# Kernel optimization log

Measured on AMD Instinct MI355X. Metric: run time of the kernel, lower is better.

Reference implementation:

```python
import jax, jax.numpy as jnp
import numpy as np
from jax import lax

N, C, A, H, W = 32, 512, 256, 64, 64

def _maxpool2(t):
    # 2x2 max pool, stride 2, NCHW
    return lax.reduce_window(t, -jnp.inf, lax.max, (1, 1, 2, 2), (1, 1, 2, 2), 'VALID')

def setup_inputs() -> dict:
    key = jax.random.key(0)
    ks = jax.random.split(key, 5)
    return {
        'x': jax.random.normal(ks[0], (N, C, H, W), dtype=jnp.float32),
        'w_g': jax.random.normal(ks[1], (A, C), dtype=jnp.float32) * 0.02,
        'b_g': jax.random.normal(ks[2], (A,), dtype=jnp.float32) * 0.02,
        'w_phi': jax.random.normal(ks[3], (A, C), dtype=jnp.float32) * 0.02,
        'b_phi': jax.random.normal(ks[4], (A,), dtype=jnp.float32) * 0.02,
    }

def reference(x, w_g, b_g, w_phi, b_phi):
    n, c, h, w = x.shape
    # g: 1x1 conv in->attn, flattened spatial: (N, A, H*W)
    g_x = (jnp.einsum('nchw,ac->nahw', x, w_g) + b_g[None, :, None, None]).reshape(n, A, h * w)
    # theta: maxpool of x, (N, C, HW/4)
    theta_x = _maxpool2(x).reshape(n, c, -1)
    # phi: 1x1 conv then maxpool, (N, HW/4, A)
    phi_conv = jnp.einsum('nchw,ac->nahw', x, w_phi) + b_phi[None, :, None, None]
    phi_x = _maxpool2(phi_conv).reshape(n, A, -1)  # (N, A, HW/4)
    # channel-attention scores: (N, C, A)
    cmat = jnp.einsum('ncm,nam->nca', theta_x, phi_x)
    attn = jax.nn.softmax(cmat, axis=-1)
    # aggregate: (N, C, HW)
    y = jnp.einsum('nca,nal->ncl', attn, g_x)
    z = y.reshape(n, c, h, w)
    return z + x
```

## Files before the change

### kernel.cpp

```cpp
#include <hip/hip_runtime.h>


typedef _Float16 half8 __attribute__((ext_vector_type(8)));
typedef _Float16 half4v __attribute__((ext_vector_type(4)));
typedef float f32x4 __attribute__((ext_vector_type(4)));

#define NB 32
#define CD 512
#define AD 256
#define PD 4096
#define PPD 1024

#define OFF_XT    0UL
#define OFF_WC    134217728UL
#define OFF_THETA 134742016UL
#define OFF_GT    168296448UL
#define OFF_PHI   235405312UL
#define OFF_ATTN  252182528UL

#define GLOAD16(gp, lp) \
    __builtin_amdgcn_global_load_lds((const __attribute__((address_space(1))) void*)(gp), \
                                     (__attribute__((address_space(3))) void*)(lp), 16, 0, 0)

__device__ __forceinline__ int swz_off(int row, int q) {
    return row * 32 + ((q ^ ((row >> 1) & 3)) * 8);
}

template <int LD>
__device__ __forceinline__ void stage2(const _Float16* __restrict__ Ab,
                                       const _Float16* __restrict__ Bb,
                                       int k0, _Float16* bufA, _Float16* bufB, int t) {
#pragma unroll
    for (int j = 0; j < 4; ++j) {
        int idx = j * 256 + t;
        int ci = idx & 511;
        int row = ci >> 2, chP = ci & 3;
        int chL = chP ^ ((row >> 1) & 3);
        const _Float16* src = ((idx < 512) ? Ab : Bb) + (size_t)row * LD + k0 + chL * 8;
        _Float16* dst = ((idx < 512) ? bufA : bufB) + ci * 8;
        GLOAD16(src, dst);
    }
}

__global__ __launch_bounds__(256) void k_prep_w(const float* __restrict__ w_g,
                                                const float* __restrict__ w_phi,
                                                _Float16* __restrict__ Wc) {
    int idx4 = blockIdx.x * 256 + threadIdx.x;
    int flat = idx4 * 4;
    const float* src = (flat < AD * CD) ? (w_g + flat) : (w_phi + (flat - AD * CD));
    float4 v = *(const float4*)src;
    half4v h;
    h[0] = (_Float16)v.x; h[1] = (_Float16)v.y; h[2] = (_Float16)v.z; h[3] = (_Float16)v.w;
    *(half4v*)(Wc + flat) = h;
}

__global__ __launch_bounds__(256) void k_prep_x(const float* __restrict__ x,
                                                _Float16* __restrict__ xT,
                                                _Float16* __restrict__ theta) {
    __shared__ _Float16 tile[32 * 136];
    int pb = blockIdx.x;
    int cb = blockIdx.y;
    int n  = blockIdx.z;
    int t  = threadIdx.x;
    int p0 = pb * 128, c0 = cb * 32;

    const float* xbase = x + ((size_t)n * CD + c0) * PD + p0;
#pragma unroll
    for (int i = 0; i < 4; ++i) {
        int idx = i * 256 + t;
        int cl = idx >> 5;
        int ch = idx & 31;
        float4 v = *(const float4*)(xbase + (size_t)cl * PD + ch * 4);
        half4v h;
        h[0] = (_Float16)v.x; h[1] = (_Float16)v.y; h[2] = (_Float16)v.z; h[3] = (_Float16)v.w;
        *(half4v*)&tile[cl * 136 + ch * 4] = h;
    }
    __syncthreads();

    {
        int pl = t >> 1, ch = t & 1;
        _Float16 vals[16] __attribute__((aligned(16)));
#pragma unroll
        for (int j = 0; j < 16; ++j) vals[j] = tile[(ch * 16 + j) * 136 + pl];
        _Float16* dst = xT + ((size_t)n * PD + p0 + pl) * CD + c0 + ch * 16;
        *(uint4*)dst       = *(uint4*)&vals[0];
        *(uint4*)(dst + 8) = *(uint4*)&vals[8];
    }
    {
        int cl = t >> 3, u0 = (t & 7) * 4;
        _Float16 o[4] __attribute__((aligned(8)));
#pragma unroll
        for (int j = 0; j < 4; ++j) {
            int w2 = (u0 + j) * 2;
            float a0 = (float)tile[cl * 136 + w2];
            float a1 = (float)tile[cl * 136 + w2 + 1];
            float a2 = (float)tile[cl * 136 + 64 + w2];
            float a3 = (float)tile[cl * 136 + 64 + w2 + 1];
            o[j] = (_Float16)fmaxf(fmaxf(a0, a1), fmaxf(a2, a3));
        }
        _Float16* dst = theta + ((size_t)n * CD + c0 + cl) * PPD + pb * 32 + u0;
        *(uint2*)dst = *(uint2*)&o[0];
    }
}

__global__ __launch_bounds__(256) void k_gemm1(const _Float16* __restrict__ Wc,
                                               const _Float16* __restrict__ xT,
                                               const float* __restrict__ b_g,
                                               const float* __restrict__ b_phi,
                                               _Float16* __restrict__ gT,
                                               _Float16* __restrict__ phi) {
    __shared__ _Float16 smem[17408];

    int pb = blockIdx.x, ab = blockIdx.y, n = blockIdx.z;
    int a0 = ab * 128, p0 = pb * 128;
    int t = threadIdx.x;
    int w = t >> 6, l = t & 63;
    int ln = l & 15, q = l >> 4;
    int mw = (w >> 1) * 64, nw = (w & 1) * 64;

    const f32x4 vzero = {0.f, 0.f, 0.f, 0.f};
    f32x4 acc[4][4];
#pragma unroll
    for (int i = 0; i < 4; ++i)
#pragma unroll
        for (int j = 0; j < 4; ++j) acc[i][j] = vzero;

    const _Float16* Abase = Wc + (size_t)a0 * CD;
    const _Float16* Bbase = xT + ((size_t)n * PD + p0) * CD;

    stage2<CD>(Abase, Bbase, 0, smem, smem + 4096, t);
    __syncthreads();

    for (int ks = 0; ks < 16; ++ks) {
        int oc = (ks & 1) << 13;
        int on = oc ^ 8192;
        if (ks < 15) stage2<CD>(Abase, Bbase, (ks + 1) * 32, smem + on, smem + on + 4096, t);
        _Float16* As = smem + oc;
        _Float16* Bs = smem + oc + 4096;
        half8 af[4], bf[4];
#pragma unroll
        for (int mt = 0; mt < 4; ++mt) af[mt] = *(const half8*)&As[swz_off(mw + mt * 16 + ln, q)];
#pragma unroll
        for (int nt = 0; nt < 4; ++nt) bf[nt] = *(const half8*)&Bs[swz_off(nw + nt * 16 + ln, q)];
#pragma unroll
        for (int mt = 0; mt < 4; ++mt)
#pragma unroll
            for (int nt = 0; nt < 4; ++nt)
                acc[mt][nt] = __builtin_amdgcn_mfma_f32_16x16x32_f16(af[mt], bf[nt], acc[mt][nt], 0, 0, 0);
        __syncthreads();
    }

    bool is_g = (a0 < 256);
    const float* bias = is_g ? b_g : b_phi;
    int abase = a0 - (is_g ? 0 : 256);
    float bv[4][4];
#pragma unroll
    for (int mt = 0; mt < 4; ++mt)
#pragma unroll
        for (int r = 0; r < 4; ++r) bv[mt][r] = bias[abase + mw + mt * 16 + q * 4 + r];

    _Float16* T = smem;
    if (is_g) {
#pragma unroll
        for (int mt = 0; mt < 4; ++mt)
#pragma unroll
            for (int nt = 0; nt < 4; ++nt)
#pragma unroll
                for (int r = 0; r < 4; ++r) {
                    int al = mw + mt * 16 + q * 4 + r;
                    int pl = nw + nt * 16 + ln;
                    T[pl * 136 + al] = (_Float16)(acc[mt][nt][r] + bv[mt][r]);
                }
        __syncthreads();
#pragma unroll
        for (int i = 0; i < 8; ++i) {
            int idx = i * 256 + t;
            int pl = idx >> 4, ch = idx & 15;
            uint4 v = *(uint4*)&T[pl * 136 + ch * 8];
            *(uint4*)(gT + ((size_t)n * PD + p0 + pl) * AD + a0 + ch * 8) = v;
        }
    } else {
#pragma unroll
        for (int mt = 0; mt < 4; ++mt)
#pragma unroll
            for (int nt = 0; nt < 4; ++nt)
#pragma unroll
                for (int r = 0; r < 4; ++r) {
                    int al = mw + mt * 16 + q * 4 + r;
                    int pl = nw + nt * 16 + ln;
                    T[al * 136 + pl] = (_Float16)(acc[mt][nt][r] + bv[mt][r]);
                }
        __syncthreads();
        int al = t >> 1, hf = t & 1;
        _Float16 o[16] __attribute__((aligned(16)));
#pragma unroll
        for (int j = 0; j < 16; ++j) {
            int u = hf * 16 + j;
            float v0 = (float)T[al * 136 + 2 * u];
            float v1 = (float)T[al * 136 + 2 * u + 1];
            float v2 = (float)T[al * 136 + 64 + 2 * u];
            float v3 = (float)T[al * 136 + 64 + 2 * u + 1];
            o[j] = (_Float16)fmaxf(fmaxf(v0, v1), fmaxf(v2, v3));
        }
        _Float16* dst = phi + ((size_t)n * AD + (a0 - 256) + al) * PPD + pb * 32 + hf * 16;
        *(uint4*)dst       = *(uint4*)&o[0];
        *(uint4*)(dst + 8) = *(uint4*)&o[8];
    }
}

__global__ __launch_bounds__(256) void k_gemm2(const _Float16* __restrict__ theta,
                                               const _Float16* __restrict__ phi,
                                               _Float16* __restrict__ attn) {
    __shared__ float red[3 * 64 * 65];
    int cb = blockIdx.x;
    int n  = blockIdx.y;
    int t = threadIdx.x, w = t >> 6, l = t & 63;
    int ln = l & 15, q = l >> 4;
    int c0 = cb * 16;

    const _Float16* Ab = theta + ((size_t)n * CD + c0 + ln) * PPD + w * 256;
    const _Float16* Bb = phi + ((size_t)n * AD + ln) * PPD + w * 256;

    const f32x4 vzero = {0.f, 0.f, 0.f, 0.f};
    f32x4 acc[16];
#pragma unroll
    for (int i = 0; i < 16; ++i) acc[i] = vzero;

    for (int k0 = 0; k0 < 256; k0 += 32) {
        half8 af = *(const half8*)(Ab + k0 + q * 8);
#pragma unroll
        for (int nt = 0; nt < 16; ++nt) {
            half8 bf = *(const half8*)(Bb + (size_t)nt * 16 * PPD + k0 + q * 8);
            acc[nt] = __builtin_amdgcn_mfma_f32_16x16x32_f16(af, bf, acc[nt], 0, 0, 0);
        }
    }

    if (w > 0) {
        float* dst = red + (w - 1) * 64 * 65 + l * 65;
#pragma unroll
        for (int nt = 0; nt < 16; ++nt)
#pragma unroll
            for (int r = 0; r < 4; ++r) dst[nt * 4 + r] = acc[nt][r];
    }
    __syncthreads();
    if (w == 0) {
#pragma unroll
        for (int j = 0; j < 3; ++j) {
            const float* src = red + j * 64 * 65 + l * 65;
#pragma unroll
            for (int nt = 0; nt < 16; ++nt)
#pragma unroll
                for (int r = 0; r < 4; ++r) acc[nt][r] += src[nt * 4 + r];
        }
#pragma unroll
        for (int r = 0; r < 4; ++r) {
            float m = -1e30f;
#pragma unroll
            for (int nt = 0; nt < 16; ++nt) m = fmaxf(m, acc[nt][r]);
#pragma unroll
            for (int s = 1; s < 16; s <<= 1) m = fmaxf(m, __shfl_xor(m, s, 64));
            float sum = 0.f;
#pragma unroll
            for (int nt = 0; nt < 16; ++nt) {
                float e = __expf(acc[nt][r] - m);
                acc[nt][r] = e;
                sum += e;
            }
#pragma unroll
            for (int s = 1; s < 16; s <<= 1) sum += __shfl_xor(sum, s, 64);
            float inv = 1.0f / sum;
            int c = c0 + q * 4 + r;
            _Float16* dst = attn + ((size_t)n * CD + c) * AD + ln;
#pragma unroll
            for (int nt = 0; nt < 16; ++nt) dst[nt * 16] = (_Float16)(acc[nt][r] * inv);
        }
    }
}

__global__ __launch_bounds__(256) void k_gemm3(const _Float16* __restrict__ attn,
                                               const _Float16* __restrict__ gT,
                                               const float* __restrict__ x,
                                               float* __restrict__ out) {
    __shared__ _Float16 smem[16384];

    int pb = blockIdx.x, cb = blockIdx.y, n = blockIdx.z;
    int c0 = cb * 128, p0 = pb * 128;
    int t = threadIdx.x;
    int w = t >> 6, l = t & 63;
    int ln = l & 15, q = l >> 4;
    int mw = (w >> 1) * 64, nw = (w & 1) * 64;

    const f32x4 vzero = {0.f, 0.f, 0.f, 0.f};
    f32x4 acc[4][4];
#pragma unroll
    for (int i = 0; i < 4; ++i)
#pragma unroll
        for (int j = 0; j < 4; ++j) acc[i][j] = vzero;

    const _Float16* Abase = attn + ((size_t)n * CD + c0) * AD;
    const _Float16* Bbase = gT + ((size_t)n * PD + p0) * AD;

    stage2<AD>(Abase, Bbase, 0, smem, smem + 4096, t);
    __syncthreads();

    for (int ks = 0; ks < 8; ++ks) {
        int oc = (ks & 1) << 13;
        int on = oc ^ 8192;
        if (ks < 7) stage2<AD>(Abase, Bbase, (ks + 1) * 32, smem + on, smem + on + 4096, t);
        _Float16* As = smem + oc;
        _Float16* Bs = smem + oc + 4096;
        half8 af[4], bf[4];
#pragma unroll
        for (int mt = 0; mt < 4; ++mt) af[mt] = *(const half8*)&Bs[swz_off(mw + mt * 16 + ln, q)];
#pragma unroll
        for (int nt = 0; nt < 4; ++nt) bf[nt] = *(const half8*)&As[swz_off(nw + nt * 16 + ln, q)];
#pragma unroll
        for (int mt = 0; mt < 4; ++mt)
#pragma unroll
            for (int nt = 0; nt < 4; ++nt)
                acc[mt][nt] = __builtin_amdgcn_mfma_f32_16x16x32_f16(af[mt], bf[nt], acc[mt][nt], 0, 0, 0);
        __syncthreads();
    }

#pragma unroll
    for (int mt = 0; mt < 4; ++mt) {
        int p = p0 + mw + mt * 16 + q * 4;
#pragma unroll
        for (int nt = 0; nt < 4; ++nt) {
            int c = c0 + nw + nt * 16 + ln;
            size_t off = ((size_t)n * CD + c) * PD + p;
            f32x4 xv = *(const f32x4*)(x + off);
            *(f32x4*)(out + off) = acc[mt][nt] + xv;
        }
    }
}

extern "C" void kernel_launch(void* const* d_in, const int* in_sizes, int n_in,
                              void* d_out, int out_size, void* d_ws, size_t ws_size,
                              hipStream_t stream) {
    const float* x     = (const float*)d_in[0];
    const float* w_g   = (const float*)d_in[1];
    const float* b_g   = (const float*)d_in[2];
    const float* w_phi = (const float*)d_in[3];
    const float* b_phi = (const float*)d_in[4];
    float* out = (float*)d_out;

    char* ws = (char*)d_ws;
    _Float16* xT    = (_Float16*)(ws + OFF_XT);
    _Float16* Wc    = (_Float16*)(ws + OFF_WC);
    _Float16* theta = (_Float16*)(ws + OFF_THETA);
    _Float16* gT    = (_Float16*)(ws + OFF_GT);
    _Float16* phi   = (_Float16*)(ws + OFF_PHI);
    _Float16* attn  = (_Float16*)(ws + OFF_ATTN);

    k_prep_w<<<dim3(256), 256, 0, stream>>>(w_g, w_phi, Wc);
    k_prep_x<<<dim3(32, 16, 32), 256, 0, stream>>>(x, xT, theta);
    k_gemm1<<<dim3(32, 4, 32), 256, 0, stream>>>(Wc, xT, b_g, b_phi, gT, phi);
    k_gemm2<<<dim3(32, 32), 256, 0, stream>>>(theta, phi, attn);
    k_gemm3<<<dim3(32, 4, 32), 256, 0, stream>>>(attn, gT, x, out);
}
```

Measured before the change: 778.6 us.

## Load GEMM operands directly from global memory instead of LDS staging

```diff
diff --git a/kernel.cpp b/kernel.cpp
--- a/kernel.cpp
+++ b/kernel.cpp
@@ -17,30 +17,6 @@
 #define OFF_GT    168296448UL
 #define OFF_PHI   235405312UL
 #define OFF_ATTN  252182528UL
-
-#define GLOAD16(gp, lp) \
-    __builtin_amdgcn_global_load_lds((const __attribute__((address_space(1))) void*)(gp), \
-                                     (__attribute__((address_space(3))) void*)(lp), 16, 0, 0)
-
-__device__ __forceinline__ int swz_off(int row, int q) {
-    return row * 32 + ((q ^ ((row >> 1) & 3)) * 8);
-}
-
-template <int LD>
-__device__ __forceinline__ void stage2(const _Float16* __restrict__ Ab,
-                                       const _Float16* __restrict__ Bb,
-                                       int k0, _Float16* bufA, _Float16* bufB, int t) {
-#pragma unroll
-    for (int j = 0; j < 4; ++j) {
-        int idx = j * 256 + t;
-        int ci = idx & 511;
-        int row = ci >> 2, chP = ci & 3;
-        int chL = chP ^ ((row >> 1) & 3);
-        const _Float16* src = ((idx < 512) ? Ab : Bb) + (size_t)row * LD + k0 + chL * 8;
-        _Float16* dst = ((idx < 512) ? bufA : bufB) + ci * 8;
-        GLOAD16(src, dst);
-    }
-}
 
 __global__ __launch_bounds__(256) void k_prep_w(const float* __restrict__ w_g,
                                                 const float* __restrict__ w_phi,
@@ -109,7 +85,7 @@
                                                const float* __restrict__ b_phi,
                                                _Float16* __restrict__ gT,
                                                _Float16* __restrict__ phi) {
-    __shared__ _Float16 smem[17408];
+    __shared__ _Float16 T[128 * 136];
 
     int pb = blockIdx.x, ab = blockIdx.y, n = blockIdx.z;
     int a0 = ab * 128, p0 = pb * 128;
@@ -125,29 +101,27 @@
 #pragma unroll
         for (int j = 0; j < 4; ++j) acc[i][j] = vzero;
 
-    const _Float16* Abase = Wc + (size_t)a0 * CD;
-    const _Float16* Bbase = xT + ((size_t)n * PD + p0) * CD;
-
-    stage2<CD>(Abase, Bbase, 0, smem, smem + 4096, t);
-    __syncthreads();
-
+    const _Float16* arow[4];
+    const _Float16* brow[4];
+#pragma unroll
+    for (int mt = 0; mt < 4; ++mt)
+        arow[mt] = Wc + (size_t)(a0 + mw + mt * 16 + ln) * CD + q * 8;
+#pragma unroll
+    for (int nt = 0; nt < 4; ++nt)
+        brow[nt] = xT + ((size_t)n * PD + p0 + nw + nt * 16 + ln) * CD + q * 8;
+
+#pragma unroll 4
     for (int ks = 0; ks < 16; ++ks) {
-        int oc = (ks & 1) << 13;
-        int on = oc ^ 8192;
-        if (ks < 15) stage2<CD>(Abase, Bbase, (ks + 1) * 32, smem + on, smem + on + 4096, t);
-        _Float16* As = smem + oc;
-        _Float16* Bs = smem + oc + 4096;
         half8 af[4], bf[4];
 #pragma unroll
-        for (int mt = 0; mt < 4; ++mt) af[mt] = *(const half8*)&As[swz_off(mw + mt * 16 + ln, q)];
-#pragma unroll
-        for (int nt = 0; nt < 4; ++nt) bf[nt] = *(const half8*)&Bs[swz_off(nw + nt * 16 + ln, q)];
+        for (int mt = 0; mt < 4; ++mt) af[mt] = *(const half8*)(arow[mt] + ks * 32);
+#pragma unroll
+        for (int nt = 0; nt < 4; ++nt) bf[nt] = *(const half8*)(brow[nt] + ks * 32);
 #pragma unroll
         for (int mt = 0; mt < 4; ++mt)
 #pragma unroll
             for (int nt = 0; nt < 4; ++nt)
                 acc[mt][nt] = __builtin_amdgcn_mfma_f32_16x16x32_f16(af[mt], bf[nt], acc[mt][nt], 0, 0, 0);
-        __syncthreads();
     }
 
     bool is_g = (a0 < 256);
@@ -159,7 +133,6 @@
 #pragma unroll
         for (int r = 0; r < 4; ++r) bv[mt][r] = bias[abase + mw + mt * 16 + q * 4 + r];
 
-    _Float16* T = smem;
     if (is_g) {
 #pragma unroll
         for (int mt = 0; mt < 4; ++mt)
@@ -281,8 +254,6 @@
                                                const _Float16* __restrict__ gT,
                                                const float* __restrict__ x,
                                                float* __restrict__ out) {
-    __shared__ _Float16 smem[16384];
-
     int pb = blockIdx.x, cb = blockIdx.y, n = blockIdx.z;
     int c0 = cb * 128, p0 = pb * 128;
     int t = threadIdx.x;
@@ -297,29 +268,27 @@
 #pragma unroll
         for (int j = 0; j < 4; ++j) acc[i][j] = vzero;
 
-    const _Float16* Abase = attn + ((size_t)n * CD + c0) * AD;
-    const _Float16* Bbase = gT + ((size_t)n * PD + p0) * AD;
-
-    stage2<AD>(Abase, Bbase, 0, smem, smem + 4096, t);
-    __syncthreads();
-
+    const _Float16* arow[4];
+    const _Float16* brow[4];
+#pragma unroll
+    for (int mt = 0; mt < 4; ++mt)
+        arow[mt] = gT + ((size_t)n * PD + p0 + mw + mt * 16 + ln) * AD + q * 8;
+#pragma unroll
+    for (int nt = 0; nt < 4; ++nt)
+        brow[nt] = attn + ((size_t)n * CD + c0 + nw + nt * 16 + ln) * AD + q * 8;
+
+#pragma unroll 4
     for (int ks = 0; ks < 8; ++ks) {
-        int oc = (ks & 1) << 13;
-        int on = oc ^ 8192;
-        if (ks < 7) stage2<AD>(Abase, Bbase, (ks + 1) * 32, smem + on, smem + on + 4096, t);
-        _Float16* As = smem + oc;
-        _Float16* Bs = smem + oc + 4096;
         half8 af[4], bf[4];
 #pragma unroll
-        for (int mt = 0; mt < 4; ++mt) af[mt] = *(const half8*)&Bs[swz_off(mw + mt * 16 + ln, q)];
-#pragma unroll
-        for (int nt = 0; nt < 4; ++nt) bf[nt] = *(const half8*)&As[swz_off(nw + nt * 16 + ln, q)];
+        for (int mt = 0; mt < 4; ++mt) af[mt] = *(const half8*)(arow[mt] + ks * 32);
+#pragma unroll
+        for (int nt = 0; nt < 4; ++nt) bf[nt] = *(const half8*)(brow[nt] + ks * 32);
 #pragma unroll
         for (int mt = 0; mt < 4; ++mt)
 #pragma unroll
             for (int nt = 0; nt < 4; ++nt)
                 acc[mt][nt] = __builtin_amdgcn_mfma_f32_16x16x32_f16(af[mt], bf[nt], acc[mt][nt], 0, 0, 0);
-        __syncthreads();
     }
 
 #pragma unroll
```

Result: slower. 940.6 us (+20.8%).

## Triple-buffer LDS staging in GEMM kernels with one barrier per k-step

Applied to the files above, without the earlier changes.

```diff
diff --git a/kernel.cpp b/kernel.cpp
--- a/kernel.cpp
+++ b/kernel.cpp
@@ -109,7 +109,7 @@
                                                const float* __restrict__ b_phi,
                                                _Float16* __restrict__ gT,
                                                _Float16* __restrict__ phi) {
-    __shared__ _Float16 smem[17408];
+    __shared__ _Float16 smem[24576];
 
     int pb = blockIdx.x, ab = blockIdx.y, n = blockIdx.z;
     int a0 = ab * 128, p0 = pb * 128;
@@ -129,12 +129,18 @@
     const _Float16* Bbase = xT + ((size_t)n * PD + p0) * CD;
 
     stage2<CD>(Abase, Bbase, 0, smem, smem + 4096, t);
-    __syncthreads();
-
-    for (int ks = 0; ks < 16; ++ks) {
-        int oc = (ks & 1) << 13;
-        int on = oc ^ 8192;
-        if (ks < 15) stage2<CD>(Abase, Bbase, (ks + 1) * 32, smem + on, smem + on + 4096, t);
+    stage2<CD>(Abase, Bbase, 32, smem + 8192, smem + 8192 + 4096, t);
+
+#pragma unroll
+    for (int ks = 0; ks < 15; ++ks) {
+        asm volatile("s_waitcnt vmcnt(4)" ::: "memory");
+        __builtin_amdgcn_s_barrier();
+        __builtin_amdgcn_sched_barrier(0);
+        if (ks + 2 < 16) {
+            int ob = ((ks + 2) % 3) * 8192;
+            stage2<CD>(Abase, Bbase, (ks + 2) * 32, smem + ob, smem + ob + 4096, t);
+        }
+        int oc = (ks % 3) * 8192;
         _Float16* As = smem + oc;
         _Float16* Bs = smem + oc + 4096;
         half8 af[4], bf[4];
@@ -147,8 +153,26 @@
 #pragma unroll
             for (int nt = 0; nt < 4; ++nt)
                 acc[mt][nt] = __builtin_amdgcn_mfma_f32_16x16x32_f16(af[mt], bf[nt], acc[mt][nt], 0, 0, 0);
-        __syncthreads();
-    }
+    }
+    asm volatile("s_waitcnt vmcnt(0)" ::: "memory");
+    __builtin_amdgcn_s_barrier();
+    __builtin_amdgcn_sched_barrier(0);
+    {
+        int oc = (15 % 3) * 8192;
+        _Float16* As = smem + oc;
+        _Float16* Bs = smem + oc + 4096;
+        half8 af[4], bf[4];
+#pragma unroll
+        for (int mt = 0; mt < 4; ++mt) af[mt] = *(const half8*)&As[swz_off(mw + mt * 16 + ln, q)];
+#pragma unroll
+        for (int nt = 0; nt < 4; ++nt) bf[nt] = *(const half8*)&Bs[swz_off(nw + nt * 16 + ln, q)];
+#pragma unroll
+        for (int mt = 0; mt < 4; ++mt)
+#pragma unroll
+            for (int nt = 0; nt < 4; ++nt)
+                acc[mt][nt] = __builtin_amdgcn_mfma_f32_16x16x32_f16(af[mt], bf[nt], acc[mt][nt], 0, 0, 0);
+    }
+    __syncthreads();
 
     bool is_g = (a0 < 256);
     const float* bias = is_g ? b_g : b_phi;
@@ -281,7 +305,7 @@
                                                const _Float16* __restrict__ gT,
                                                const float* __restrict__ x,
                                                float* __restrict__ out) {
-    __shared__ _Float16 smem[16384];
+    __shared__ _Float16 smem[24576];
 
     int pb = blockIdx.x, cb = blockIdx.y, n = blockIdx.z;
     int c0 = cb * 128, p0 = pb * 128;
@@ -301,12 +325,18 @@
     const _Float16* Bbase = gT + ((size_t)n * PD + p0) * AD;
 
     stage2<AD>(Abase, Bbase, 0, smem, smem + 4096, t);
-    __syncthreads();
-
-    for (int ks = 0; ks < 8; ++ks) {
-        int oc = (ks & 1) << 13;
-        int on = oc ^ 8192;
-        if (ks < 7) stage2<AD>(Abase, Bbase, (ks + 1) * 32, smem + on, smem + on + 4096, t);
+    stage2<AD>(Abase, Bbase, 32, smem + 8192, smem + 8192 + 4096, t);
+
+#pragma unroll
+    for (int ks = 0; ks < 7; ++ks) {
+        asm volatile("s_waitcnt vmcnt(4)" ::: "memory");
+        __builtin_amdgcn_s_barrier();
+        __builtin_amdgcn_sched_barrier(0);
+        if (ks + 2 < 8) {
+            int ob = ((ks + 2) % 3) * 8192;
+            stage2<AD>(Abase, Bbase, (ks + 2) * 32, smem + ob, smem + ob + 4096, t);
+        }
+        int oc = (ks % 3) * 8192;
         _Float16* As = smem + oc;
         _Float16* Bs = smem + oc + 4096;
         half8 af[4], bf[4];
@@ -319,18 +349,41 @@
 #pragma unroll
             for (int nt = 0; nt < 4; ++nt)
                 acc[mt][nt] = __builtin_amdgcn_mfma_f32_16x16x32_f16(af[mt], bf[nt], acc[mt][nt], 0, 0, 0);
-        __syncthreads();
+    }
+    asm volatile("s_waitcnt vmcnt(0)" ::: "memory");
+    __builtin_amdgcn_s_barrier();
+    __builtin_amdgcn_sched_barrier(0);
+    {
+        int oc = (7 % 3) * 8192;
+        _Float16* As = smem + oc;
+        _Float16* Bs = smem + oc + 4096;
+        half8 af[4], bf[4];
+#pragma unroll
+        for (int mt = 0; mt < 4; ++mt) af[mt] = *(const half8*)&Bs[swz_off(mw + mt * 16 + ln, q)];
+#pragma unroll
+        for (int nt = 0; nt < 4; ++nt) bf[nt] = *(const half8*)&As[swz_off(nw + nt * 16 + ln, q)];
+#pragma unroll
+        for (int mt = 0; mt < 4; ++mt)
+#pragma unroll
+            for (int nt = 0; nt < 4; ++nt)
+                acc[mt][nt] = __builtin_amdgcn_mfma_f32_16x16x32_f16(af[mt], bf[nt], acc[mt][nt], 0, 0, 0);
     }
 
 #pragma unroll
     for (int mt = 0; mt < 4; ++mt) {
         int p = p0 + mw + mt * 16 + q * 4;
+        size_t offs[4];
+        f32x4 xv[4];
 #pragma unroll
         for (int nt = 0; nt < 4; ++nt) {
             int c = c0 + nw + nt * 16 + ln;
-            size_t off = ((size_t)n * CD + c) * PD + p;
-            f32x4 xv = *(const f32x4*)(x + off);
-            *(f32x4*)(out + off) = acc[mt][nt] + xv;
+            offs[nt] = ((size_t)n * CD + c) * PD + p;
+            xv[nt] = __builtin_nontemporal_load((const f32x4*)(x + offs[nt]));
+        }
+#pragma unroll
+        for (int nt = 0; nt < 4; ++nt) {
+            f32x4 r = acc[mt][nt] + xv[nt];
+            __builtin_nontemporal_store(r, (f32x4*)(out + offs[nt]));
         }
     }
 }
```

Result: no change. 776.7 us (-0.2%).

## Fuse x transpose/theta pooling into first GEMM with full-K LDS panel

Applied to the files above, without the earlier changes.

```diff
diff --git a/kernel.cpp b/kernel.cpp
--- a/kernel.cpp
+++ b/kernel.cpp
@@ -11,7 +11,6 @@
 #define PD 4096
 #define PPD 1024
 
-#define OFF_XT    0UL
 #define OFF_WC    134217728UL
 #define OFF_THETA 134742016UL
 #define OFF_GT    168296448UL
@@ -54,69 +53,53 @@
     *(half4v*)(Wc + flat) = h;
 }
 
-__global__ __launch_bounds__(256) void k_prep_x(const float* __restrict__ x,
-                                                _Float16* __restrict__ xT,
-                                                _Float16* __restrict__ theta) {
-    __shared__ _Float16 tile[32 * 136];
-    int pb = blockIdx.x;
-    int cb = blockIdx.y;
-    int n  = blockIdx.z;
-    int t  = threadIdx.x;
-    int p0 = pb * 128, c0 = cb * 32;
-
-    const float* xbase = x + ((size_t)n * CD + c0) * PD + p0;
-#pragma unroll
-    for (int i = 0; i < 4; ++i) {
-        int idx = i * 256 + t;
-        int cl = idx >> 5;
-        int ch = idx & 31;
-        float4 v = *(const float4*)(xbase + (size_t)cl * PD + ch * 4);
-        half4v h;
-        h[0] = (_Float16)v.x; h[1] = (_Float16)v.y; h[2] = (_Float16)v.z; h[3] = (_Float16)v.w;
-        *(half4v*)&tile[cl * 136 + ch * 4] = h;
-    }
-    __syncthreads();
-
-    {
-        int pl = t >> 1, ch = t & 1;
-        _Float16 vals[16] __attribute__((aligned(16)));
-#pragma unroll
-        for (int j = 0; j < 16; ++j) vals[j] = tile[(ch * 16 + j) * 136 + pl];
-        _Float16* dst = xT + ((size_t)n * PD + p0 + pl) * CD + c0 + ch * 16;
-        *(uint4*)dst       = *(uint4*)&vals[0];
-        *(uint4*)(dst + 8) = *(uint4*)&vals[8];
-    }
-    {
-        int cl = t >> 3, u0 = (t & 7) * 4;
-        _Float16 o[4] __attribute__((aligned(8)));
-#pragma unroll
-        for (int j = 0; j < 4; ++j) {
-            int w2 = (u0 + j) * 2;
-            float a0 = (float)tile[cl * 136 + w2];
-            float a1 = (float)tile[cl * 136 + w2 + 1];
-            float a2 = (float)tile[cl * 136 + 64 + w2];
-            float a3 = (float)tile[cl * 136 + 64 + w2 + 1];
-            o[j] = (_Float16)fmaxf(fmaxf(a0, a1), fmaxf(a2, a3));
-        }
-        _Float16* dst = theta + ((size_t)n * CD + c0 + cl) * PPD + pb * 32 + u0;
-        *(uint2*)dst = *(uint2*)&o[0];
-    }
-}
-
-__global__ __launch_bounds__(256) void k_gemm1(const _Float16* __restrict__ Wc,
-                                               const _Float16* __restrict__ xT,
-                                               const float* __restrict__ b_g,
-                                               const float* __restrict__ b_phi,
-                                               _Float16* __restrict__ gT,
-                                               _Float16* __restrict__ phi) {
-    __shared__ _Float16 smem[17408];
-
-    int pb = blockIdx.x, ab = blockIdx.y, n = blockIdx.z;
-    int a0 = ab * 128, p0 = pb * 128;
+__global__ __launch_bounds__(1024) void k_gemm1f(const _Float16* __restrict__ Wc,
+                                                 const float* __restrict__ x,
+                                                 const float* __restrict__ b_g,
+                                                 const float* __restrict__ b_phi,
+                                                 _Float16* __restrict__ gT,
+                                                 _Float16* __restrict__ phi,
+                                                 _Float16* __restrict__ theta) {
+    __shared__ _Float16 smem[70912];
+    _Float16* panel = smem;
+    _Float16* tile1 = smem + 66560;
+
+    int pb = blockIdx.x, n = blockIdx.y;
+    int p0 = pb * 128;
     int t = threadIdx.x;
     int w = t >> 6, l = t & 63;
     int ln = l & 15, q = l >> 4;
-    int mw = (w >> 1) * 64, nw = (w & 1) * 64;
+    int wa = w >> 1, wp = w & 1;
+    int a0w = wa * 64, p0w = wp * 64;
+
+    for (int s = 0; s < 16; ++s) {
+        int c0 = s * 32;
+        {
+            int cl = t >> 5, ch = t & 31;
+            float4 v = *(const float4*)(x + ((size_t)n * CD + c0 + cl) * PD + p0 + ch * 4);
+            half4v h;
+            h[0] = (_Float16)v.x; h[1] = (_Float16)v.y; h[2] = (_Float16)v.z; h[3] = (_Float16)v.w;
+            *(half4v*)&tile1[cl * 136 + ch * 4] = h;
+        }
+        __syncthreads();
+        {
+            int pl = t >> 3, co = (t & 7) * 4;
+            _Float16 vals[4] __attribute__((aligned(8)));
+#pragma unroll
+            for (int j = 0; j < 4; ++j) vals[j] = tile1[(co + j) * 136 + pl];
+            *(uint2*)&panel[pl * 520 + c0 + co] = *(uint2*)&vals[0];
+        }
+        {
+            int cl = t >> 5, u = t & 31;
+            float a0 = (float)tile1[cl * 136 + 2 * u];
+            float a1 = (float)tile1[cl * 136 + 2 * u + 1];
+            float a2 = (float)tile1[cl * 136 + 64 + 2 * u];
+            float a3 = (float)tile1[cl * 136 + 64 + 2 * u + 1];
+            theta[((size_t)n * CD + c0 + cl) * PPD + pb * 32 + u] =
+                (_Float16)fmaxf(fmaxf(a0, a1), fmaxf(a2, a3));
+        }
+        __syncthreads();
+    }
 
     const f32x4 vzero = {0.f, 0.f, 0.f, 0.f};
     f32x4 acc[4][4];
@@ -125,41 +108,51 @@
 #pragma unroll
         for (int j = 0; j < 4; ++j) acc[i][j] = vzero;
 
-    const _Float16* Abase = Wc + (size_t)a0 * CD;
-    const _Float16* Bbase = xT + ((size_t)n * PD + p0) * CD;
-
-    stage2<CD>(Abase, Bbase, 0, smem, smem + 4096, t);
+    const _Float16* arow = Wc + (size_t)(a0w + ln) * CD + q * 8;
+    const _Float16* prow = panel + (p0w + ln) * 520 + q * 8;
+
+    half8 afA[4], afB[4], bf[4];
+#pragma unroll
+    for (int mt = 0; mt < 4; ++mt) afA[mt] = *(const half8*)(arow + mt * 16 * CD);
+
+#pragma unroll
+    for (int ks2 = 0; ks2 < 8; ++ks2) {
+        int kA = 2 * ks2, kB = 2 * ks2 + 1;
+#pragma unroll
+        for (int mt = 0; mt < 4; ++mt) afB[mt] = *(const half8*)(arow + mt * 16 * CD + kB * 32);
+#pragma unroll
+        for (int nt = 0; nt < 4; ++nt) bf[nt] = *(const half8*)(prow + nt * 16 * 520 + kA * 32);
+#pragma unroll
+        for (int mt = 0; mt < 4; ++mt)
+#pragma unroll
+            for (int nt = 0; nt < 4; ++nt)
+                acc[mt][nt] = __builtin_amdgcn_mfma_f32_16x16x32_f16(afA[mt], bf[nt], acc[mt][nt], 0, 0, 0);
+        if (kB < 15) {
+#pragma unroll
+            for (int mt = 0; mt < 4; ++mt) afA[mt] = *(const half8*)(arow + mt * 16 * CD + (kB + 1) * 32);
+        }
+#pragma unroll
+        for (int nt = 0; nt < 4; ++nt) bf[nt] = *(const half8*)(prow + nt * 16 * 520 + kB * 32);
+#pragma unroll
+        for (int mt = 0; mt < 4; ++mt)
+#pragma unroll
+            for (int nt = 0; nt < 4; ++nt)
+                acc[mt][nt] = __builtin_amdgcn_mfma_f32_16x16x32_f16(afB[mt], bf[nt], acc[mt][nt], 0, 0, 0);
+    }
+
     __syncthreads();
 
-    for (int ks = 0; ks < 16; ++ks) {
-        int oc = (ks & 1) << 13;
-        int on = oc ^ 8192;
-        if (ks < 15) stage2<CD>(Abase, Bbase, (ks + 1) * 32, smem + on, smem + on + 4096, t);
-        _Float16* As = smem + oc;
-        _Float16* Bs = smem + oc + 4096;
-        half8 af[4], bf[4];
-#pragma unroll
-        for (int mt = 0; mt < 4; ++mt) af[mt] = *(const half8*)&As[swz_off(mw + mt * 16 + ln, q)];
-#pragma unroll
-        for (int nt = 0; nt < 4; ++nt) bf[nt] = *(const half8*)&Bs[swz_off(nw + nt * 16 + ln, q)];
-#pragma unroll
-        for (int mt = 0; mt < 4; ++mt)
-#pragma unroll
-            for (int nt = 0; nt < 4; ++nt)
-                acc[mt][nt] = __builtin_amdgcn_mfma_f32_16x16x32_f16(af[mt], bf[nt], acc[mt][nt], 0, 0, 0);
-        __syncthreads();
-    }
-
-    bool is_g = (a0 < 256);
+    bool is_g = (wa < 4);
     const float* bias = is_g ? b_g : b_phi;
-    int abase = a0 - (is_g ? 0 : 256);
+    int ab0 = a0w - (is_g ? 0 : 256);
     float bv[4][4];
 #pragma unroll
     for (int mt = 0; mt < 4; ++mt)
 #pragma unroll
-        for (int r = 0; r < 4; ++r) bv[mt][r] = bias[abase + mw + mt * 16 + q * 4 + r];
-
-    _Float16* T = smem;
+        for (int r = 0; r < 4; ++r) bv[mt][r] = bias[ab0 + mt * 16 + q * 4 + r];
+
+    _Float16* Tg = smem;
+    _Float16* Tp = smem + 33792;
     if (is_g) {
 #pragma unroll
         for (int mt = 0; mt < 4; ++mt)
@@ -167,18 +160,10 @@
             for (int nt = 0; nt < 4; ++nt)
 #pragma unroll
                 for (int r = 0; r < 4; ++r) {
-                    int al = mw + mt * 16 + q * 4 + r;
-                    int pl = nw + nt * 16 + ln;
-                    T[pl * 136 + al] = (_Float16)(acc[mt][nt][r] + bv[mt][r]);
+                    int al = a0w + mt * 16 + q * 4 + r;
+                    int pl = p0w + nt * 16 + ln;
+                    Tg[pl * 264 + al] = (_Float16)(acc[mt][nt][r] + bv[mt][r]);
                 }
-        __syncthreads();
-#pragma unroll
-        for (int i = 0; i < 8; ++i) {
-            int idx = i * 256 + t;
-            int pl = idx >> 4, ch = idx & 15;
-            uint4 v = *(uint4*)&T[pl * 136 + ch * 8];
-            *(uint4*)(gT + ((size_t)n * PD + p0 + pl) * AD + a0 + ch * 8) = v;
-        }
     } else {
 #pragma unroll
         for (int mt = 0; mt < 4; ++mt)
@@ -186,25 +171,33 @@
             for (int nt = 0; nt < 4; ++nt)
 #pragma unroll
                 for (int r = 0; r < 4; ++r) {
-                    int al = mw + mt * 16 + q * 4 + r;
-                    int pl = nw + nt * 16 + ln;
-                    T[al * 136 + pl] = (_Float16)(acc[mt][nt][r] + bv[mt][r]);
+                    int al = (a0w - 256) + mt * 16 + q * 4 + r;
+                    int pl = p0w + nt * 16 + ln;
+                    Tp[al * 136 + pl] = (_Float16)(acc[mt][nt][r] + bv[mt][r]);
                 }
-        __syncthreads();
-        int al = t >> 1, hf = t & 1;
-        _Float16 o[16] __attribute__((aligned(16)));
-#pragma unroll
-        for (int j = 0; j < 16; ++j) {
-            int u = hf * 16 + j;
-            float v0 = (float)T[al * 136 + 2 * u];
-            float v1 = (float)T[al * 136 + 2 * u + 1];
-            float v2 = (float)T[al * 136 + 64 + 2 * u];
-            float v3 = (float)T[al * 136 + 64 + 2 * u + 1];
+    }
+    __syncthreads();
+
+#pragma unroll
+    for (int i = 0; i < 4; ++i) {
+        int idx = i * 1024 + t;
+        int pl = idx >> 5, ch = idx & 31;
+        uint4 v = *(uint4*)&Tg[pl * 264 + ch * 8];
+        *(uint4*)(gT + ((size_t)n * PD + p0 + pl) * AD + ch * 8) = v;
+    }
+    {
+        int al = t >> 2, u0 = (t & 3) * 8;
+        _Float16 o[8] __attribute__((aligned(16)));
+#pragma unroll
+        for (int j = 0; j < 8; ++j) {
+            int u = u0 + j;
+            float v0 = (float)Tp[al * 136 + 2 * u];
+            float v1 = (float)Tp[al * 136 + 2 * u + 1];
+            float v2 = (float)Tp[al * 136 + 64 + 2 * u];
+            float v3 = (float)Tp[al * 136 + 64 + 2 * u + 1];
             o[j] = (_Float16)fmaxf(fmaxf(v0, v1), fmaxf(v2, v3));
         }
-        _Float16* dst = phi + ((size_t)n * AD + (a0 - 256) + al) * PPD + pb * 32 + hf * 16;
-        *(uint4*)dst       = *(uint4*)&o[0];
-        *(uint4*)(dst + 8) = *(uint4*)&o[8];
+        *(uint4*)(phi + ((size_t)n * AD + al) * PPD + pb * 32 + u0) = *(uint4*)&o[0];
     }
 }
 
@@ -322,17 +315,20 @@
         __syncthreads();
     }
 
-#pragma unroll
-    for (int mt = 0; mt < 4; ++mt) {
-        int p = p0 + mw + mt * 16 + q * 4;
+    size_t ebase = ((size_t)n * CD + c0 + nw + ln) * PD + (size_t)(p0 + mw + q * 4);
+    f32x4 xv[4][4];
+#pragma unroll
+    for (int mt = 0; mt < 4; ++mt)
+#pragma unroll
+        for (int nt = 0; nt < 4; ++nt)
+            xv[mt][nt] = *(const f32x4*)(x + ebase + (size_t)nt * 16 * PD + mt * 16);
+#pragma unroll
+    for (int mt = 0; mt < 4; ++mt)
 #pragma unroll
         for (int nt = 0; nt < 4; ++nt) {
-            int c = c0 + nw + nt * 16 + ln;
-            size_t off = ((size_t)n * CD + c) * PD + p;
-            f32x4 xv = *(const f32x4*)(x + off);
-            *(f32x4*)(out + off) = acc[mt][nt] + xv;
-        }
-    }
+            f32x4 r = acc[mt][nt] + xv[mt][nt];
+            __builtin_nontemporal_store(r, (f32x4*)(out + ebase + (size_t)nt * 16 * PD + mt * 16));
+        }
 }
 
 extern "C" void kernel_launch(void* const* d_in, const int* in_sizes, int n_in,
@@ -346,7 +342,6 @@
     float* out = (float*)d_out;
 
     char* ws = (char*)d_ws;
-    _Float16* xT    = (_Float16*)(ws + OFF_XT);
     _Float16* Wc    = (_Float16*)(ws + OFF_WC);
     _Float16* theta = (_Float16*)(ws + OFF_THETA);
     _Float16* gT    = (_Float16*)(ws + OFF_GT);
@@ -354,8 +349,7 @@
     _Float16* attn  = (_Float16*)(ws + OFF_ATTN);
 
     k_prep_w<<<dim3(256), 256, 0, stream>>>(w_g, w_phi, Wc);
-    k_prep_x<<<dim3(32, 16, 32), 256, 0, stream>>>(x, xT, theta);
-    k_gemm1<<<dim3(32, 4, 32), 256, 0, stream>>>(Wc, xT, b_g, b_phi, gT, phi);
+    k_gemm1f<<<dim3(32, 32), 1024, 0, stream>>>(Wc, x, b_g, b_phi, gT, phi, theta);
     k_gemm2<<<dim3(32, 32), 256, 0, stream>>>(theta, phi, attn);
     k_gemm3<<<dim3(32, 4, 32), 256, 0, stream>>>(attn, gT, x, out);
 }
```

Result: faster. 748.5 us (-3.9%).
